# Performance work log

Measured on AMD Instinct MI355X. Metric: run time of the kernel, lower is better.

## Reference

```python
import jax, jax.numpy as jnp
import numpy as np

H = W = 256
WS = 8          # window size
SHIFT = 4       # shift size
HEADS = 8
DIM = 128
HD = DIM // HEADS
EPS = 1e-5


def _rel_index():
    # Swin-style relative position index, static constant (N=WS*WS)
    coords = np.stack(np.meshgrid(np.arange(WS), np.arange(WS), indexing='ij')).reshape(2, -1)
    rel = coords[:, :, None] - coords[:, None, :]        # (2, N, N)
    rel = rel + (WS - 1)
    return rel[0] * (2 * WS - 1) + rel[1]                # (N, N) in [0, (2WS-1)^2)

_REL_IDX = _rel_index()


def _ln(x, w, b):
    m = jnp.mean(x, axis=-1, keepdims=True)
    v = jnp.var(x, axis=-1, keepdims=True)
    return (x - m) * jax.lax.rsqrt(v + EPS) * w + b


def setup_inputs() -> dict:
    key = jax.random.key(0)
    ks = jax.random.split(key, 8)
    s = 0.02
    return {
        'x': jax.random.normal(ks[0], (2, H * W, DIM), jnp.float32),
        'norm1_w': jnp.ones((DIM,), jnp.float32),
        'norm1_b': jnp.zeros((DIM,), jnp.float32),
        'qkv_w': jax.random.normal(ks[1], (3 * DIM, DIM), jnp.float32) * s,
        'qkv_b': jnp.zeros((3 * DIM,), jnp.float32),
        'rel_bias_table': jax.random.normal(ks[2], ((2 * WS - 1) ** 2, HEADS), jnp.float32) * s,
        'proj_w': jax.random.normal(ks[3], (DIM, DIM), jnp.float32) * s,
        'proj_b': jnp.zeros((DIM,), jnp.float32),
        'norm2_w': jnp.ones((DIM,), jnp.float32),
        'norm2_b': jnp.zeros((DIM,), jnp.float32),
        'fc1_w': jax.random.normal(ks[4], (4 * DIM, DIM), jnp.float32) * s,
        'fc1_b': jnp.zeros((4 * DIM,), jnp.float32),
        'fc2_w': jax.random.normal(ks[5], (DIM, 4 * DIM), jnp.float32) * s,
        'fc2_b': jnp.zeros((DIM,), jnp.float32),
    }


def reference(x, norm1_w, norm1_b, qkv_w, qkv_b, rel_bias_table, proj_w, proj_b,
              norm2_w, norm2_b, fc1_w, fc1_b, fc2_w, fc2_b):
    B, L, C = x.shape
    N = WS * WS
    shortcut = x

    # norm1 -> spatial -> shift (roll only; original applies no attention mask)
    xs = _ln(x, norm1_w, norm1_b).reshape(B, H, W, C)
    xs = jnp.roll(xs, shift=(-SHIFT, -SHIFT), axis=(1, 2))

    # window partition: (B*nH*nW, N, C)
    win = xs.reshape(B, H // WS, WS, W // WS, WS, C)
    win = win.transpose(0, 1, 3, 2, 4, 5).reshape(-1, N, C)

    # window attention
    qkv = (win @ qkv_w.T + qkv_b).reshape(-1, N, 3, HEADS, HD)
    qkv = qkv.transpose(2, 0, 3, 1, 4)                   # (3, nWin, heads, N, hd)
    q, k, v = qkv[0], qkv[1], qkv[2]
    scale = HD ** -0.5
    attn = jnp.einsum('whnd,whmd->whnm', q * scale, k)   # (nWin, heads, N, N)
    bias = rel_bias_table[_REL_IDX]                      # (N, N, heads)
    attn = attn + bias.transpose(2, 0, 1)[None]
    attn = jax.nn.softmax(attn, axis=-1)
    out = jnp.einsum('whnm,whmd->whnd', attn, v)         # (nWin, heads, N, hd)
    out = out.transpose(0, 2, 1, 3).reshape(-1, N, C)
    out = out @ proj_w.T + proj_b

    # window reverse + un-shift
    out = out.reshape(B, H // WS, W // WS, WS, WS, C)
    out = out.transpose(0, 1, 3, 2, 4, 5).reshape(B, H, W, C)
    out = jnp.roll(out, shift=(SHIFT, SHIFT), axis=(1, 2)).reshape(B, L, C)

    x = shortcut + out

    # MLP (fc1 -> exact GELU -> fc2) with residual
    h = _ln(x, norm2_w, norm2_b)
    h = jax.nn.gelu(h @ fc1_w.T + fc1_b, approximate=False)
    h = h @ fc2_w.T + fc2_b
    return x + h
```

## Files before the change

kernel.cpp:

```cpp
#include <hip/hip_runtime.h>
#include <hip/hip_bf16.h>
#include <cmath>

#define LNEPS 1e-5f

typedef __attribute__((ext_vector_type(8))) short short8v;
typedef __attribute__((ext_vector_type(4))) float f32x4;

__device__ __forceinline__ unsigned short f2bf(float f){
  unsigned u = __float_as_uint(f);
  u += 0x7fffu + ((u >> 16) & 1u);
  return (unsigned short)(u >> 16);
}
template <int P>
__device__ __forceinline__ void setprio(){
#ifdef __HIP_DEVICE_COMPILE__
  __builtin_amdgcn_s_setprio(P);
#endif
}
__device__ __forceinline__ float frcp(float x){
#ifdef __HIP_DEVICE_COMPILE__
  return __builtin_amdgcn_rcpf(x);
#else
  return 1.f / x;
#endif
}
__device__ __forceinline__ float gelu_s(float x){
  return x * frcp(1.f + __expf(-1.702f * x));
}

__device__ __forceinline__ f32x4 mfma32(short8v a, short8v b, f32x4 c){
#ifdef __HIP_DEVICE_COMPILE__
  return __builtin_amdgcn_mfma_f32_16x16x32_bf16(a, b, c, 0, 0, 0);
#else
  return c;
#endif
}

__device__ __forceinline__ void stage128(const unsigned short* g, int ldg, short* lds){
#ifdef __HIP_DEVICE_COMPILE__
  const int t = threadIdx.x;
  const int wv = t >> 6;
  #pragma unroll
  for (int it = 0; it < 8; ++it) {
    const int flat = it * 256 + t;
    const int r = flat >> 4, c = flat & 15;
    const unsigned short* src = g + (size_t)r * ldg + ((c ^ (r & 7)) << 3);
    short* dst = lds + (size_t)(it * 256 + wv * 64) * 8;
    __builtin_amdgcn_global_load_lds(
        (const __attribute__((address_space(1))) void*)src,
        (__attribute__((address_space(3))) void*)dst, 16, 0, 0);
  }
#else
  (void)g; (void)ldg; (void)lds;
#endif
}
__device__ __forceinline__ void stage64(const unsigned short* g, short* lds){
#ifdef __HIP_DEVICE_COMPILE__
  const int t = threadIdx.x;
  const int wv = t >> 6;
  #pragma unroll
  for (int it = 0; it < 4; ++it) {
    const int flat = it * 256 + t;
    const int r = flat >> 4, c = flat & 15;
    const unsigned short* src = g + (size_t)r * 128 + ((c ^ (r & 7)) << 3);
    short* dst = lds + (size_t)(it * 256 + wv * 64) * 8;
    __builtin_amdgcn_global_load_lds(
        (const __attribute__((address_space(1))) void*)src,
        (__attribute__((address_space(3))) void*)dst, 16, 0, 0);
  }
#else
  (void)g; (void)lds;
#endif
}
__device__ __forceinline__ short8v frag_ld(const short* lds, int row, int chunk){
  return *(const short8v*)((const char*)lds + row * 256 + ((chunk ^ (row & 7)) << 4));
}

__global__ __launch_bounds__(256) void k0_cvt(
    const float* __restrict__ qkvw, const float* __restrict__ pw,
    const float* __restrict__ w1, const float* __restrict__ w2,
    const float* __restrict__ table,
    unsigned short* __restrict__ dst, float* __restrict__ be)
{
  if (blockIdx.x < 192) {
    const int i = (blockIdx.x * 256 + threadIdx.x) * 4;
    const float* src; int off;
    if (i < 49152)       { src = qkvw; off = i; }
    else if (i < 65536)  { src = pw;   off = i - 49152; }
    else if (i < 131072) { src = w1;   off = i - 65536; }
    else                 { src = w2;   off = i - 131072; }
    const float4 v = *(const float4*)(src + off);
    ushort4 o = { f2bf(v.x), f2bf(v.y), f2bf(v.z), f2bf(v.w) };
    *(ushort4*)(dst + i) = o;
  } else {
    const int i = (blockIdx.x - 192) * 256 + threadIdx.x;
    const int m4 = (i & 15) * 4;
    const int r  = (i >> 4) & 63;
    const int h  = i >> 10;
    const int i1 = r >> 3, j1 = r & 7;
    float o[4];
    #pragma unroll
    for (int e = 0; e < 4; ++e) {
      const int m = m4 + e;
      const int i2 = m >> 3, j2 = m & 7;
      o[e] = table[((i1 - i2 + 7) * 15 + (j1 - j2 + 7)) * 8 + h];
    }
    float4 ov = { o[0], o[1], o[2], o[3] };
    *(float4*)(be + ((h * 64 + r) * 64 + m4)) = ov;
  }
}

__global__ __launch_bounds__(256, 2) void k23_qkv_attn(
    const float* __restrict__ x,
    const float* __restrict__ gw, const float* __restrict__ gb,
    const unsigned short* __restrict__ Wb,
    const float* __restrict__ bias,
    const float* __restrict__ be,
    unsigned short* __restrict__ attn)
{
  __shared__ __align__(16) short At[128 * 128];
  __shared__ __align__(16) short Bt[64 * 128];
  __shared__ __align__(16) short QK[64 * 256];
  const int t = threadIdx.x;
  const int win = blockIdx.x;
  const int row0 = win * 64;
  stage128(Wb, 128, At);
  #pragma unroll
  for (int it = 0; it < 4; ++it) {
    const int flat = it * 256 + t;
    const int r = flat >> 4, c = flat & 15;
    const int row = row0 + r;
    const int wid = row >> 6, n = row & 63;
    const int b = wid >> 10, rem = wid & 1023;
    const int wh = rem >> 5, wwi = rem & 31;
    const int i2 = n >> 3, j2 = n & 7;
    const int sh = (wh * 8 + i2 + 4) & 255;
    const int sw = (wwi * 8 + j2 + 4) & 255;
    const float* src = x + (((size_t)b << 16) + sh * 256 + sw) * 128 + c * 8;
    const float4 a0 = *(const float4*)src;
    const float4 a1 = *(const float4*)(src + 4);
    float s  = a0.x + a0.y + a0.z + a0.w + a1.x + a1.y + a1.z + a1.w;
    float ss = a0.x*a0.x + a0.y*a0.y + a0.z*a0.z + a0.w*a0.w
             + a1.x*a1.x + a1.y*a1.y + a1.z*a1.z + a1.w*a1.w;
    s += __shfl_xor(s, 1); ss += __shfl_xor(ss, 1);
    s += __shfl_xor(s, 2); ss += __shfl_xor(ss, 2);
    s += __shfl_xor(s, 4); ss += __shfl_xor(ss, 4);
    s += __shfl_xor(s, 8); ss += __shfl_xor(ss, 8);
    const float mean = s * 0.0078125f;
    const float rstd = rsqrtf(ss * 0.0078125f - mean * mean + LNEPS);
    const float4 g0 = *(const float4*)(gw + c * 8), g1 = *(const float4*)(gw + c * 8 + 4);
    const float4 c0 = *(const float4*)(gb + c * 8), c1 = *(const float4*)(gb + c * 8 + 4);
    uint4 pk;
    pk.x = (unsigned)f2bf((a0.x - mean) * rstd * g0.x + c0.x)
         | ((unsigned)f2bf((a0.y - mean) * rstd * g0.y + c0.y) << 16);
    pk.y = (unsigned)f2bf((a0.z - mean) * rstd * g0.z + c0.z)
         | ((unsigned)f2bf((a0.w - mean) * rstd * g0.w + c0.w) << 16);
    pk.z = (unsigned)f2bf((a1.x - mean) * rstd * g1.x + c1.x)
         | ((unsigned)f2bf((a1.y - mean) * rstd * g1.y + c1.y) << 16);
    pk.w = (unsigned)f2bf((a1.z - mean) * rstd * g1.z + c1.z)
         | ((unsigned)f2bf((a1.w - mean) * rstd * g1.w + c1.w) << 16);
    *(uint4*)((char*)Bt + r * 256 + ((c ^ (r & 7)) << 4)) = pk;
  }
  __syncthreads();

  const int l = t & 63, w = t >> 6, w0 = w & 1, w1 = w >> 1;
  const int g = l >> 4, rl = l & 15;
  const f32x4 z = {0.f, 0.f, 0.f, 0.f};

  for (int nt = 0; nt < 3; ++nt) {
    f32x4 acc[4][2];
    #pragma unroll
    for (int i = 0; i < 4; ++i) { acc[i][0] = z; acc[i][1] = z; }
    #pragma unroll
    for (int kk = 0; kk < 4; ++kk) {
      short8v a[4], b[2];
      #pragma unroll
      for (int i = 0; i < 4; ++i) a[i] = frag_ld(At, w0 * 64 + i * 16 + rl, kk * 4 + g);
      #pragma unroll
      for (int j = 0; j < 2; ++j) b[j] = frag_ld(Bt, w1 * 32 + j * 16 + rl, kk * 4 + g);
      #pragma unroll
      for (int i = 0; i < 4; ++i)
        #pragma unroll
        for (int j = 0; j < 2; ++j)
          acc[i][j] = mfma32(a[i], b[j], acc[i][j]);
    }
    if (nt < 2) {
      __syncthreads();
      stage128(Wb + (size_t)(nt + 1) * 16384, 128, At);
      #pragma unroll
      for (int i = 0; i < 4; ++i) {
        const int c = w0 * 64 + i * 16 + 4 * g;
        const float4 bv = *(const float4*)(bias + nt * 128 + c);
        const int chunk = nt * 16 + (c >> 3), inner = (c & 7) * 2;
        #pragma unroll
        for (int j = 0; j < 2; ++j) {
          const int r = w1 * 32 + j * 16 + rl;
          ushort4 o = { f2bf(acc[i][j][0] + bv.x), f2bf(acc[i][j][1] + bv.y),
                        f2bf(acc[i][j][2] + bv.z), f2bf(acc[i][j][3] + bv.w) };
          *(ushort4*)((char*)QK + r * 512 + ((chunk ^ (r & 7)) << 4) + inner) = o;
        }
      }
      __syncthreads();
    } else {
      __syncthreads();
      #pragma unroll
      for (int i = 0; i < 4; ++i) {
        const int c = w0 * 64 + i * 16 + 4 * g;
        const int h2 = c >> 4, db = c & 15;
        const float4 bv = *(const float4*)(bias + 256 + c);
        const float ba[4] = {bv.x, bv.y, bv.z, bv.w};
        #pragma unroll
        for (int j = 0; j < 2; ++j) {
          const int m = w1 * 32 + j * 16 + rl;
          char* vb = (char*)Bt + h2 * 2048;
          #pragma unroll
          for (int e = 0; e < 4; ++e) {
            const int d = db + e;
            *(unsigned short*)(vb + d * 128 + (((m >> 3) ^ (d & 7)) << 4) + (m & 7) * 2)
                = f2bf(acc[i][j][e] + ba[e]);
          }
        }
      }
      __syncthreads();
    }
  }

  char* Pw = (char*)At + w * 4096;
  const short8v zz = {0,0,0,0,0,0,0,0};
  for (int hh = 0; hh < 2; ++hh) {
    const int h = w * 2 + hh;
    short8v qf[4], kf[4];
    if (g < 2) {
      #pragma unroll
      for (int rf = 0; rf < 4; ++rf) {
        const int r = rf * 16 + rl;
        qf[rf] = *(const short8v*)((char*)QK + r * 512 + (((2 * h + g) ^ (r & 7)) << 4));
      }
      #pragma unroll
      for (int mf = 0; mf < 4; ++mf) {
        const int r = mf * 16 + rl;
        kf[mf] = *(const short8v*)((char*)QK + r * 512 + (((16 + 2 * h + g) ^ (r & 7)) << 4));
      }
    } else {
      #pragma unroll
      for (int i = 0; i < 4; ++i) { qf[i] = zz; kf[i] = zz; }
    }
    f32x4 s[4][4];
    #pragma unroll
    for (int mf = 0; mf < 4; ++mf)
      #pragma unroll
      for (int rf = 0; rf < 4; ++rf)
        s[mf][rf] = mfma32(kf[mf], qf[rf], z);
    float sum[4];
    #pragma unroll
    for (int rf = 0; rf < 4; ++rf) {
      const int r = rf * 16 + rl;
      const float* bp = be + (size_t)(h * 64 + r) * 64;
      float mx = -1e30f;
      #pragma unroll
      for (int mf = 0; mf < 4; ++mf) {
        const float4 bv = *(const float4*)(bp + mf * 16 + g * 4);
        const float ba[4] = {bv.x, bv.y, bv.z, bv.w};
        #pragma unroll
        for (int e = 0; e < 4; ++e) {
          const float v = s[mf][rf][e] * 0.25f + ba[e];
          s[mf][rf][e] = v;
          mx = fmaxf(mx, v);
        }
      }
      mx = fmaxf(mx, __shfl_xor(mx, 16));
      mx = fmaxf(mx, __shfl_xor(mx, 32));
      float sm = 0.f;
      #pragma unroll
      for (int mf = 0; mf < 4; ++mf)
        #pragma unroll
        for (int e = 0; e < 4; ++e) {
          const float ev = __expf(s[mf][rf][e] - mx);
          s[mf][rf][e] = ev;
          sm += ev;
        }
      sm += __shfl_xor(sm, 16);
      sm += __shfl_xor(sm, 32);
      sum[rf] = sm;
    }
    const char* vbase = (char*)Bt + h * 2048;
    f32x4 o[4];
    #pragma unroll
    for (int rf = 0; rf < 4; ++rf) o[rf] = z;
    #pragma unroll
    for (int hm = 0; hm < 2; ++hm) {
      #pragma unroll
      for (int rf = 0; rf < 4; ++rf) {
        const int r = rf * 16 + rl;
        #pragma unroll
        for (int mfl = 0; mfl < 2; ++mfl) {
          const int mf = hm * 2 + mfl;
          uint2 u;
          u.x = (unsigned)f2bf(s[mf][rf][0]) | ((unsigned)f2bf(s[mf][rf][1]) << 16);
          u.y = (unsigned)f2bf(s[mf][rf][2]) | ((unsigned)f2bf(s[mf][rf][3]) << 16);
          *(uint2*)(Pw + r * 64 + (((mfl * 2 + (g >> 1)) ^ ((r >> 1) & 3)) << 4) + (g & 1) * 8) = u;
        }
      }
      const short8v va = *(const short8v*)(vbase + rl * 128 + (((hm * 4 + g) ^ (rl & 7)) << 4));
      #pragma unroll
      for (int rf = 0; rf < 4; ++rf) {
        const int r = rf * 16 + rl;
        const short8v pb = *(const short8v*)(Pw + r * 64 + ((g ^ ((r >> 1) & 3)) << 4));
        o[rf] = mfma32(va, pb, o[rf]);
      }
    }
    #pragma unroll
    for (int rf = 0; rf < 4; ++rf) {
      const float inv = 1.f / sum[rf];
      const int r = rf * 16 + rl;
      ushort4 ov = { f2bf(o[rf][0] * inv), f2bf(o[rf][1] * inv),
                     f2bf(o[rf][2] * inv), f2bf(o[rf][3] * inv) };
      *(ushort4*)(attn + ((size_t)win * 64 + r) * 128 + h * 16 + g * 4) = ov;
    }
  }
}

__global__ __launch_bounds__(256, 2) void k45_proj_mlp(
    const unsigned short* __restrict__ A,
    const unsigned short* __restrict__ pwb,
    const float* __restrict__ pb,
    const float* __restrict__ xin,
    const float* __restrict__ gw, const float* __restrict__ gb,
    const unsigned short* __restrict__ w1b, const float* __restrict__ b1,
    const unsigned short* __restrict__ w2b, const float* __restrict__ b2,
    float* __restrict__ out)
{
  __shared__ __align__(16) short Xt[64 * 128];
  __shared__ __align__(16) short Ht[64 * 128];
  __shared__ __align__(16) short Wt[128 * 128];
  __shared__ float2 Red[64 * 8];
  const int t = threadIdx.x;
  const int row0 = blockIdx.x * 64;
  stage128(pwb, 128, Wt);
  stage64(A + (size_t)row0 * 128, Ht);
  const int l = t & 63, w = t >> 6, w0 = w & 1, w1 = w >> 1;
  const int g = l >> 4, rl = l & 15;
  size_t obase[2];
  float4 xv[4][2];
  #pragma unroll
  for (int j = 0; j < 2; ++j) {
    const int r = row0 + w1 * 32 + j * 16 + rl;
    const int wn = r >> 6, n = r & 63;
    const int b_ = wn >> 10, rem = wn & 1023;
    const int wh = rem >> 5, ww = rem & 31;
    const int si = n >> 3, sj = n & 7;
    const int hd = (wh * 8 + si + 4) & 255;
    const int wd = (ww * 8 + sj + 4) & 255;
    obase[j] = (((size_t)b_ << 16) + hd * 256 + wd) * 128;
    #pragma unroll
    for (int i = 0; i < 4; ++i)
      xv[i][j] = *(const float4*)(xin + obase[j] + w0 * 64 + i * 16 + 4 * g);
  }
  __syncthreads();
  const f32x4 z = {0.f, 0.f, 0.f, 0.f};
  f32x4 x2r[4][2];
  #pragma unroll
  for (int i = 0; i < 4; ++i) { x2r[i][0] = z; x2r[i][1] = z; }
  setprio<1>();
  #pragma unroll
  for (int kk = 0; kk < 4; ++kk) {
    short8v a[4], b[2];
    #pragma unroll
    for (int i = 0; i < 4; ++i) a[i] = frag_ld(Wt, w0 * 64 + i * 16 + rl, kk * 4 + g);
    #pragma unroll
    for (int j = 0; j < 2; ++j) b[j] = frag_ld(Ht, w1 * 32 + j * 16 + rl, kk * 4 + g);
    #pragma unroll
    for (int i = 0; i < 4; ++i)
      #pragma unroll
      for (int j = 0; j < 2; ++j)
        x2r[i][j] = mfma32(a[i], b[j], x2r[i][j]);
  }
  setprio<0>();
  #pragma unroll
  for (int i = 0; i < 4; ++i) {
    const float4 bv = *(const float4*)(pb + w0 * 64 + i * 16 + 4 * g);
    #pragma unroll
    for (int j = 0; j < 2; ++j) {
      x2r[i][j][0] += xv[i][j].x + bv.x;
      x2r[i][j][1] += xv[i][j].y + bv.y;
      x2r[i][j][2] += xv[i][j].z + bv.z;
      x2r[i][j][3] += xv[i][j].w + bv.w;
    }
  }
  #pragma unroll
  for (int j = 0; j < 2; ++j) {
    float s = 0.f, ss = 0.f;
    #pragma unroll
    for (int i = 0; i < 4; ++i)
      #pragma unroll
      for (int e = 0; e < 4; ++e) { const float v = x2r[i][j][e]; s += v; ss += v * v; }
    Red[(w1 * 32 + j * 16 + rl) * 8 + (w0 * 4 + g)] = make_float2(s, ss);
  }
  __syncthreads();
  stage128(w1b, 128, Wt);
  float mean[2], rstd[2];
  #pragma unroll
  for (int j = 0; j < 2; ++j) {
    const float2* rp = &Red[(w1 * 32 + j * 16 + rl) * 8];
    float s = 0.f, ss = 0.f;
    #pragma unroll
    for (int k = 0; k < 8; ++k) { s += rp[k].x; ss += rp[k].y; }
    mean[j] = s * 0.0078125f;
    rstd[j] = rsqrtf(ss * 0.0078125f - mean[j] * mean[j] + LNEPS);
  }
  #pragma unroll
  for (int i = 0; i < 4; ++i) {
    const int c = w0 * 64 + i * 16 + 4 * g;
    const float4 g4 = *(const float4*)(gw + c);
    const float4 c4 = *(const float4*)(gb + c);
    #pragma unroll
    for (int j = 0; j < 2; ++j) {
      const int r = w1 * 32 + j * 16 + rl;
      ushort4 p;
      p.x = f2bf((x2r[i][j][0] - mean[j]) * rstd[j] * g4.x + c4.x);
      p.y = f2bf((x2r[i][j][1] - mean[j]) * rstd[j] * g4.y + c4.y);
      p.z = f2bf((x2r[i][j][2] - mean[j]) * rstd[j] * g4.z + c4.z);
      p.w = f2bf((x2r[i][j][3] - mean[j]) * rstd[j] * g4.w + c4.w);
      const int chunk = c >> 3, inner = (c & 7) * 2;
      *(ushort4*)((char*)Xt + r * 256 + ((chunk ^ (r & 7)) << 4) + inner) = p;
    }
  }
  f32x4 oacc[4][2];
  #pragma unroll
  for (int i = 0; i < 4; ++i) { oacc[i][0] = z; oacc[i][1] = z; }
  for (int sb = 0; sb < 4; ++sb) {
    __syncthreads();
    if (sb > 0) {
      stage128(w1b + (size_t)sb * 16384, 128, Wt);
      __syncthreads();
    }
    f32x4 hacc[4][2];
    #pragma unroll
    for (int i = 0; i < 4; ++i) { hacc[i][0] = z; hacc[i][1] = z; }
    setprio<1>();
    #pragma unroll
    for (int kk = 0; kk < 4; ++kk) {
      short8v a[4], b[2];
      #pragma unroll
      for (int i = 0; i < 4; ++i) a[i] = frag_ld(Wt, w0 * 64 + i * 16 + rl, kk * 4 + g);
      #pragma unroll
      for (int j = 0; j < 2; ++j) b[j] = frag_ld(Xt, w1 * 32 + j * 16 + rl, kk * 4 + g);
      #pragma unroll
      for (int i = 0; i < 4; ++i)
        #pragma unroll
        for (int j = 0; j < 2; ++j)
          hacc[i][j] = mfma32(a[i], b[j], hacc[i][j]);
    }
    setprio<0>();
    __syncthreads();
    stage128(w2b + (size_t)sb * 128, 512, Wt);
    #pragma unroll
    for (int i = 0; i < 4; ++i) {
      const int cl = w0 * 64 + i * 16 + 4 * g;
      const float4 b1v = *(const float4*)(b1 + sb * 128 + cl);
      const float ba[4] = {b1v.x, b1v.y, b1v.z, b1v.w};
      #pragma unroll
      for (int j = 0; j < 2; ++j) {
        const int r = w1 * 32 + j * 16 + rl;
        ushort4 p;
        p.x = f2bf(gelu_s(hacc[i][j][0] + ba[0]));
        p.y = f2bf(gelu_s(hacc[i][j][1] + ba[1]));
        p.z = f2bf(gelu_s(hacc[i][j][2] + ba[2]));
        p.w = f2bf(gelu_s(hacc[i][j][3] + ba[3]));
        const int chunk = cl >> 3, inner = (cl & 7) * 2;
        *(ushort4*)((char*)Ht + r * 256 + ((chunk ^ (r & 7)) << 4) + inner) = p;
      }
    }
    __syncthreads();
    setprio<1>();
    #pragma unroll
    for (int kk = 0; kk < 4; ++kk) {
      short8v a[4], b[2];
      #pragma unroll
      for (int i = 0; i < 4; ++i) a[i] = frag_ld(Wt, w0 * 64 + i * 16 + rl, kk * 4 + g);
      #pragma unroll
      for (int j = 0; j < 2; ++j) b[j] = frag_ld(Ht, w1 * 32 + j * 16 + rl, kk * 4 + g);
      #pragma unroll
      for (int i = 0; i < 4; ++i)
        #pragma unroll
        for (int j = 0; j < 2; ++j)
          oacc[i][j] = mfma32(a[i], b[j], oacc[i][j]);
    }
    setprio<0>();
  }
  #pragma unroll
  for (int i = 0; i < 4; ++i) {
    const int c = w0 * 64 + i * 16 + 4 * g;
    const float4 bv = *(const float4*)(b2 + c);
    #pragma unroll
    for (int j = 0; j < 2; ++j) {
      float4 o = { x2r[i][j][0] + oacc[i][j][0] + bv.x,
                   x2r[i][j][1] + oacc[i][j][1] + bv.y,
                   x2r[i][j][2] + oacc[i][j][2] + bv.z,
                   x2r[i][j][3] + oacc[i][j][3] + bv.w };
      *(float4*)(out + obase[j] + c) = o;
    }
  }
}

extern "C" void kernel_launch(void* const* d_in, const int* in_sizes, int n_in,
                              void* d_out, int out_size, void* d_ws, size_t ws_size,
                              hipStream_t stream)
{
  const float* x    = (const float*)d_in[0];
  const float* n1w  = (const float*)d_in[1];
  const float* n1b  = (const float*)d_in[2];
  const float* qkvw = (const float*)d_in[3];
  const float* qkvB = (const float*)d_in[4];
  const float* relb = (const float*)d_in[5];
  const float* pw   = (const float*)d_in[6];
  const float* pb   = (const float*)d_in[7];
  const float* n2w  = (const float*)d_in[8];
  const float* n2b  = (const float*)d_in[9];
  const float* w1   = (const float*)d_in[10];
  const float* b1   = (const float*)d_in[11];
  const float* w2   = (const float*)d_in[12];
  const float* b2   = (const float*)d_in[13];
  float* out = (float*)d_out;

  unsigned short* winb = (unsigned short*)d_ws;
  unsigned short* wb   = winb + 16777216;
  unsigned short* qkvw_b = wb;
  unsigned short* pw_b   = wb + 49152;
  unsigned short* w1_b   = wb + 65536;
  unsigned short* w2_b   = wb + 131072;
  float* be = (float*)(wb + 196608);

  k0_cvt<<<224, 256, 0, stream>>>(qkvw, pw, w1, w2, relb, wb, be);
  k23_qkv_attn<<<2048, 256, 0, stream>>>(x, n1w, n1b, qkvw_b, qkvB, be, winb);
  k45_proj_mlp<<<2048, 256, 0, stream>>>(winb, pw_b, pb, x, n2w, n2b,
                                         w1_b, b1, w2_b, b2, out);
}
```

Baseline: 162.2 us.

## Fuse window attention and proj+MLP kernels into one per-window kernel

Merges the QKV/attention kernel and the projection/MLP kernel into a single kernel per 64-token window. The attention output stays in LDS (written swizzled into the QK buffer) instead of round-tripping through a bf16 global workspace, which removes a 32 MB write plus read and one kernel launch. LDS buffers are unified into one 80 KB pool and reused across stages, and the attention output is held in registers across a barrier. The costs are a longer kernel with higher register pressure and LDS use that may limit occupancy to fewer blocks per CU.

```diff
diff --git a/kernel.cpp b/kernel.cpp
--- a/kernel.cpp
+++ b/kernel.cpp
@@ -53,24 +53,6 @@
   }
 #else
   (void)g; (void)ldg; (void)lds;
-#endif
-}
-__device__ __forceinline__ void stage64(const unsigned short* g, short* lds){
-#ifdef __HIP_DEVICE_COMPILE__
-  const int t = threadIdx.x;
-  const int wv = t >> 6;
-  #pragma unroll
-  for (int it = 0; it < 4; ++it) {
-    const int flat = it * 256 + t;
-    const int r = flat >> 4, c = flat & 15;
-    const unsigned short* src = g + (size_t)r * 128 + ((c ^ (r & 7)) << 3);
-    short* dst = lds + (size_t)(it * 256 + wv * 64) * 8;
-    __builtin_amdgcn_global_load_lds(
-        (const __attribute__((address_space(1))) void*)src,
-        (__attribute__((address_space(3))) void*)dst, 16, 0, 0);
-  }
-#else
-  (void)g; (void)lds;
 #endif
 }
 __device__ __forceinline__ short8v frag_ld(const short* lds, int row, int chunk){
@@ -111,21 +93,26 @@
   }
 }
 
-__global__ __launch_bounds__(256, 2) void k23_qkv_attn(
+__global__ __launch_bounds__(256, 2) void k2345(
     const float* __restrict__ x,
-    const float* __restrict__ gw, const float* __restrict__ gb,
-    const unsigned short* __restrict__ Wb,
-    const float* __restrict__ bias,
+    const float* __restrict__ g1w, const float* __restrict__ g1b,
+    const unsigned short* __restrict__ qkvWb, const float* __restrict__ qkvB,
     const float* __restrict__ be,
-    unsigned short* __restrict__ attn)
+    const unsigned short* __restrict__ pwb, const float* __restrict__ pb,
+    const float* __restrict__ g2w, const float* __restrict__ g2b,
+    const unsigned short* __restrict__ w1b, const float* __restrict__ b1,
+    const unsigned short* __restrict__ w2b, const float* __restrict__ b2,
+    float* __restrict__ out)
 {
-  __shared__ __align__(16) short At[128 * 128];
-  __shared__ __align__(16) short Bt[64 * 128];
-  __shared__ __align__(16) short QK[64 * 256];
+  __shared__ __align__(16) char LP[81920];
+  short* At = (short*)LP;
+  short* Bt = (short*)(LP + 32768);
+  short* QK = (short*)(LP + 49152);
+  float2* Red = (float2*)(LP + 65536);
   const int t = threadIdx.x;
   const int win = blockIdx.x;
   const int row0 = win * 64;
-  stage128(Wb, 128, At);
+  stage128(qkvWb, 128, At);
   #pragma unroll
   for (int it = 0; it < 4; ++it) {
     const int flat = it * 256 + t;
@@ -149,8 +136,8 @@
     s += __shfl_xor(s, 8); ss += __shfl_xor(ss, 8);
     const float mean = s * 0.0078125f;
     const float rstd = rsqrtf(ss * 0.0078125f - mean * mean + LNEPS);
-    const float4 g0 = *(const float4*)(gw + c * 8), g1 = *(const float4*)(gw + c * 8 + 4);
-    const float4 c0 = *(const float4*)(gb + c * 8), c1 = *(const float4*)(gb + c * 8 + 4);
+    const float4 g0 = *(const float4*)(g1w + c * 8), g1 = *(const float4*)(g1w + c * 8 + 4);
+    const float4 c0 = *(const float4*)(g1b + c * 8), c1 = *(const float4*)(g1b + c * 8 + 4);
     uint4 pk;
     pk.x = (unsigned)f2bf((a0.x - mean) * rstd * g0.x + c0.x)
          | ((unsigned)f2bf((a0.y - mean) * rstd * g0.y + c0.y) << 16);
@@ -187,11 +174,11 @@
     }
     if (nt < 2) {
       __syncthreads();
-      stage128(Wb + (size_t)(nt + 1) * 16384, 128, At);
+      stage128(qkvWb + (size_t)(nt + 1) * 16384, 128, At);
       #pragma unroll
       for (int i = 0; i < 4; ++i) {
         const int c = w0 * 64 + i * 16 + 4 * g;
-        const float4 bv = *(const float4*)(bias + nt * 128 + c);
+        const float4 bv = *(const float4*)(qkvB + nt * 128 + c);
         const int chunk = nt * 16 + (c >> 3), inner = (c & 7) * 2;
         #pragma unroll
         for (int j = 0; j < 2; ++j) {
@@ -208,7 +195,7 @@
       for (int i = 0; i < 4; ++i) {
         const int c = w0 * 64 + i * 16 + 4 * g;
         const int h2 = c >> 4, db = c & 15;
-        const float4 bv = *(const float4*)(bias + 256 + c);
+        const float4 bv = *(const float4*)(qkvB + 256 + c);
         const float ba[4] = {bv.x, bv.y, bv.z, bv.w};
         #pragma unroll
         for (int j = 0; j < 2; ++j) {
@@ -228,6 +215,7 @@
 
   char* Pw = (char*)At + w * 4096;
   const short8v zz = {0,0,0,0,0,0,0,0};
+  f32x4 o2[2][4];
   for (int hh = 0; hh < 2; ++hh) {
     const int h = w * 2 + hh;
     short8v qf[4], kf[4];
@@ -306,41 +294,33 @@
       #pragma unroll
       for (int rf = 0; rf < 4; ++rf) {
         const int r = rf * 16 + rl;
-        const short8v pb = *(const short8v*)(Pw + r * 64 + ((g ^ ((r >> 1) & 3)) << 4));
-        o[rf] = mfma32(va, pb, o[rf]);
+        const short8v pbv = *(const short8v*)(Pw + r * 64 + ((g ^ ((r >> 1) & 3)) << 4));
+        o[rf] = mfma32(va, pbv, o[rf]);
       }
     }
     #pragma unroll
     for (int rf = 0; rf < 4; ++rf) {
       const float inv = 1.f / sum[rf];
+      o2[hh][rf][0] = o[rf][0] * inv; o2[hh][rf][1] = o[rf][1] * inv;
+      o2[hh][rf][2] = o[rf][2] * inv; o2[hh][rf][3] = o[rf][3] * inv;
+    }
+  }
+
+  __syncthreads();
+  stage128(pwb, 128, At);
+  short* Ht = QK;
+  #pragma unroll
+  for (int hh = 0; hh < 2; ++hh) {
+    const int h = w * 2 + hh;
+    const int chunk = h * 2 + (g >> 1), inner = (g & 1) * 8;
+    #pragma unroll
+    for (int rf = 0; rf < 4; ++rf) {
       const int r = rf * 16 + rl;
-      ushort4 ov = { f2bf(o[rf][0] * inv), f2bf(o[rf][1] * inv),
-                     f2bf(o[rf][2] * inv), f2bf(o[rf][3] * inv) };
-      *(ushort4*)(attn + ((size_t)win * 64 + r) * 128 + h * 16 + g * 4) = ov;
-    }
-  }
-}
-
-__global__ __launch_bounds__(256, 2) void k45_proj_mlp(
-    const unsigned short* __restrict__ A,
-    const unsigned short* __restrict__ pwb,
-    const float* __restrict__ pb,
-    const float* __restrict__ xin,
-    const float* __restrict__ gw, const float* __restrict__ gb,
-    const unsigned short* __restrict__ w1b, const float* __restrict__ b1,
-    const unsigned short* __restrict__ w2b, const float* __restrict__ b2,
-    float* __restrict__ out)
-{
-  __shared__ __align__(16) short Xt[64 * 128];
-  __shared__ __align__(16) short Ht[64 * 128];
-  __shared__ __align__(16) short Wt[128 * 128];
-  __shared__ float2 Red[64 * 8];
-  const int t = threadIdx.x;
-  const int row0 = blockIdx.x * 64;
-  stage128(pwb, 128, Wt);
-  stage64(A + (size_t)row0 * 128, Ht);
-  const int l = t & 63, w = t >> 6, w0 = w & 1, w1 = w >> 1;
-  const int g = l >> 4, rl = l & 15;
+      ushort4 ov = { f2bf(o2[hh][rf][0]), f2bf(o2[hh][rf][1]),
+                     f2bf(o2[hh][rf][2]), f2bf(o2[hh][rf][3]) };
+      *(ushort4*)((char*)Ht + r * 256 + ((chunk ^ (r & 7)) << 4) + inner) = ov;
+    }
+  }
   size_t obase[2];
   float4 xv[4][2];
   #pragma unroll
@@ -355,10 +335,10 @@
     obase[j] = (((size_t)b_ << 16) + hd * 256 + wd) * 128;
     #pragma unroll
     for (int i = 0; i < 4; ++i)
-      xv[i][j] = *(const float4*)(xin + obase[j] + w0 * 64 + i * 16 + 4 * g);
+      xv[i][j] = *(const float4*)(x + obase[j] + w0 * 64 + i * 16 + 4 * g);
   }
   __syncthreads();
-  const f32x4 z = {0.f, 0.f, 0.f, 0.f};
+
   f32x4 x2r[4][2];
   #pragma unroll
   for (int i = 0; i < 4; ++i) { x2r[i][0] = z; x2r[i][1] = z; }
@@ -367,7 +347,7 @@
   for (int kk = 0; kk < 4; ++kk) {
     short8v a[4], b[2];
     #pragma unroll
-    for (int i = 0; i < 4; ++i) a[i] = frag_ld(Wt, w0 * 64 + i * 16 + rl, kk * 4 + g);
+    for (int i = 0; i < 4; ++i) a[i] = frag_ld(At, w0 * 64 + i * 16 + rl, kk * 4 + g);
     #pragma unroll
     for (int j = 0; j < 2; ++j) b[j] = frag_ld(Ht, w1 * 32 + j * 16 + rl, kk * 4 + g);
     #pragma unroll
@@ -398,7 +378,7 @@
     Red[(w1 * 32 + j * 16 + rl) * 8 + (w0 * 4 + g)] = make_float2(s, ss);
   }
   __syncthreads();
-  stage128(w1b, 128, Wt);
+  stage128(w1b, 128, At);
   float mean[2], rstd[2];
   #pragma unroll
   for (int j = 0; j < 2; ++j) {
@@ -412,8 +392,8 @@
   #pragma unroll
   for (int i = 0; i < 4; ++i) {
     const int c = w0 * 64 + i * 16 + 4 * g;
-    const float4 g4 = *(const float4*)(gw + c);
-    const float4 c4 = *(const float4*)(gb + c);
+    const float4 g4 = *(const float4*)(g2w + c);
+    const float4 c4 = *(const float4*)(g2b + c);
     #pragma unroll
     for (int j = 0; j < 2; ++j) {
       const int r = w1 * 32 + j * 16 + rl;
@@ -423,7 +403,7 @@
       p.z = f2bf((x2r[i][j][2] - mean[j]) * rstd[j] * g4.z + c4.z);
       p.w = f2bf((x2r[i][j][3] - mean[j]) * rstd[j] * g4.w + c4.w);
       const int chunk = c >> 3, inner = (c & 7) * 2;
-      *(ushort4*)((char*)Xt + r * 256 + ((chunk ^ (r & 7)) << 4) + inner) = p;
+      *(ushort4*)((char*)Bt + r * 256 + ((chunk ^ (r & 7)) << 4) + inner) = p;
     }
   }
   f32x4 oacc[4][2];
@@ -432,7 +412,7 @@
   for (int sb = 0; sb < 4; ++sb) {
     __syncthreads();
     if (sb > 0) {
-      stage128(w1b + (size_t)sb * 16384, 128, Wt);
+      stage128(w1b + (size_t)sb * 16384, 128, At);
       __syncthreads();
     }
     f32x4 hacc[4][2];
@@ -443,9 +423,9 @@
     for (int kk = 0; kk < 4; ++kk) {
       short8v a[4], b[2];
       #pragma unroll
-      for (int i = 0; i < 4; ++i) a[i] = frag_ld(Wt, w0 * 64 + i * 16 + rl, kk * 4 + g);
-      #pragma unroll
-      for (int j = 0; j < 2; ++j) b[j] = frag_ld(Xt, w1 * 32 + j * 16 + rl, kk * 4 + g);
+      for (int i = 0; i < 4; ++i) a[i] = frag_ld(At, w0 * 64 + i * 16 + rl, kk * 4 + g);
+      #pragma unroll
+      for (int j = 0; j < 2; ++j) b[j] = frag_ld(Bt, w1 * 32 + j * 16 + rl, kk * 4 + g);
       #pragma unroll
       for (int i = 0; i < 4; ++i)
         #pragma unroll
@@ -454,7 +434,7 @@
     }
     setprio<0>();
     __syncthreads();
-    stage128(w2b + (size_t)sb * 128, 512, Wt);
+    stage128(w2b + (size_t)sb * 128, 512, At);
     #pragma unroll
     for (int i = 0; i < 4; ++i) {
       const int cl = w0 * 64 + i * 16 + 4 * g;
@@ -478,7 +458,7 @@
     for (int kk = 0; kk < 4; ++kk) {
       short8v a[4], b[2];
       #pragma unroll
-      for (int i = 0; i < 4; ++i) a[i] = frag_ld(Wt, w0 * 64 + i * 16 + rl, kk * 4 + g);
+      for (int i = 0; i < 4; ++i) a[i] = frag_ld(At, w0 * 64 + i * 16 + rl, kk * 4 + g);
       #pragma unroll
       for (int j = 0; j < 2; ++j) b[j] = frag_ld(Ht, w1 * 32 + j * 16 + rl, kk * 4 + g);
       #pragma unroll
@@ -524,8 +504,7 @@
   const float* b2   = (const float*)d_in[13];
   float* out = (float*)d_out;
 
-  unsigned short* winb = (unsigned short*)d_ws;
-  unsigned short* wb   = winb + 16777216;
+  unsigned short* wb = (unsigned short*)d_ws;
   unsigned short* qkvw_b = wb;
   unsigned short* pw_b   = wb + 49152;
   unsigned short* w1_b   = wb + 65536;
@@ -533,7 +512,6 @@
   float* be = (float*)(wb + 196608);
 
   k0_cvt<<<224, 256, 0, stream>>>(qkvw, pw, w1, w2, relb, wb, be);
-  k23_qkv_attn<<<2048, 256, 0, stream>>>(x, n1w, n1b, qkvw_b, qkvB, be, winb);
-  k45_proj_mlp<<<2048, 256, 0, stream>>>(winb, pw_b, pb, x, n2w, n2b,
-                                         w1_b, b1, w2_b, b2, out);
-}
+  k2345<<<2048, 256, 0, stream>>>(x, n1w, n1b, qkvw_b, qkvB, be,
+                                  pw_b, pb, n2w, n2b, w1_b, b1, w2_b, b2, out);
+}
```

After: 150.3 us. 1.08x faster.
